# Kernel tuning notes

Measured on AMD Instinct MI355X. Metric: run time of the kernel, lower is better.

## Reference

```python
import jax, jax.numpy as jnp
import numpy as np

DIM, M_DIM, FOURIER, KNN = 128, 16, 4, 32
EDGE_IN = 2 * FOURIER + 2 * DIM + 1  # 265


def silu(x):
    return x * jax.nn.sigmoid(x)


def setup_inputs() -> dict:
    key = jax.random.key(0)
    ks = jax.random.split(key, 12)
    b, n = 2, 4096

    def w(k, shape):
        return jax.random.normal(k, shape, dtype=jnp.float32) * 0.02

    return {
        "feats": jax.random.normal(ks[0], (b, n, DIM), dtype=jnp.float32),
        "coors": jax.random.normal(ks[1], (b, n, 3), dtype=jnp.float32) * 3.0,
        # edge_mlp: Linear(265, 530) -> SiLU -> Linear(530, 16) -> SiLU
        "We1": w(ks[2], (EDGE_IN, 2 * EDGE_IN)), "be1": jnp.zeros((2 * EDGE_IN,), jnp.float32),
        "We2": w(ks[3], (2 * EDGE_IN, M_DIM)), "be2": jnp.zeros((M_DIM,), jnp.float32),
        # coors_mlp: Linear(16, 64) -> SiLU -> Linear(64, 1)
        "Wc1": w(ks[4], (M_DIM, 4 * M_DIM)), "bc1": jnp.zeros((4 * M_DIM,), jnp.float32),
        "Wc2": w(ks[5], (4 * M_DIM, 1)), "bc2": jnp.zeros((1,), jnp.float32),
        # node_mlp: Linear(dim+16, 2*dim) -> SiLU -> Linear(2*dim, dim)
        "Wn1": w(ks[6], (DIM + M_DIM, 2 * DIM)), "bn1": jnp.zeros((2 * DIM,), jnp.float32),
        "Wn2": w(ks[7], (2 * DIM, DIM)), "bn2": jnp.zeros((DIM,), jnp.float32),
    }


def reference(feats, coors, We1, be1, We2, be2, Wc1, bc1, Wc2, bc2, Wn1, bn1, Wn2, bn2):
    b, n, d = feats.shape
    # pairwise relative coords and squared distance: (b, n, n, 3), (b, n, n)
    rel_coors = coors[:, :, None, :] - coors[:, None, :, :]
    rel_dist = jnp.sum(rel_coors ** 2, axis=-1)

    # k nearest neighbors (smallest distance)
    _, idx = jax.lax.top_k(-rel_dist, KNN)  # (b, n, K)
    rel_coors = jnp.take_along_axis(rel_coors, idx[..., None], axis=2)  # (b, n, K, 3)
    rel_dist = jnp.take_along_axis(rel_dist, idx, axis=2)[..., None]    # (b, n, K, 1)

    # fourier encode distance -> (b, n, K, 2*F + 1)
    scales = 2.0 ** jnp.arange(FOURIER, dtype=rel_dist.dtype)
    xs = rel_dist[..., None] / scales  # (b, n, K, 1, F)
    fe = jnp.concatenate([jnp.sin(xs), jnp.cos(xs), rel_dist[..., None]], axis=-1)
    rel_dist = fe.reshape(b, n, KNN, 2 * FOURIER + 1)

    bidx = jnp.arange(b)[:, None, None]
    feats_j = feats[bidx, idx]                                   # (b, n, K, d)
    feats_i = jnp.broadcast_to(feats[:, :, None, :], (b, n, KNN, d))

    edge_in = jnp.concatenate([feats_i, feats_j, rel_dist], axis=-1)  # (b, n, K, 265)
    m_ij = silu(silu(edge_in @ We1 + be1) @ We2 + be2)                # (b, n, K, m)

    coor_w = (silu(m_ij @ Wc1 + bc1) @ Wc2 + bc2)[..., 0]             # (b, n, K)
    coors_out = jnp.einsum('bij,bijc->bic', coor_w, rel_coors) + coors

    m_i = m_ij.sum(axis=2)                                            # (b, n, m)
    node_h = silu(jnp.concatenate([feats, m_i], axis=-1) @ Wn1 + bn1)
    node_out = node_h @ Wn2 + bn2 + feats
    return node_out, coors_out
```

## Files before the change

kernel.cpp:

```cpp
#include <hip/hip_runtime.h>
#include <hip/hip_bf16.h>
#include <stdint.h>

typedef __hip_bfloat16 bf16;

using sh8    = __attribute__((ext_vector_type(8)))  short;
using sh4    = __attribute__((ext_vector_type(4)))  short;
using us4    = __attribute__((ext_vector_type(4)))  unsigned short;
using f32x16 = __attribute__((ext_vector_type(16))) float;
using fx4    = __attribute__((ext_vector_type(4)))  float;
using i32x2  = __attribute__((ext_vector_type(2)))  int;

#define NN    4096
#define NODES 8192
#define DIM   128
#define MD    16
#define KNNK  32
#define H1N   530
#define CPAD  544
#define PROW  1088

#define OFF_W1AB 0
#define OFF_WE2A 8704
#define OFF_WC1A 17536
#define OFF_BE2  19584
#define OFF_BC1  19616
#define OFF_WC2  19744
#define OFF_BC2  19872
#define WIMG_SH  19880

__device__ __forceinline__ float b2f(bf16 x){ return __bfloat162float(x); }
__device__ __forceinline__ bf16  f2b(float x){ return __float2bfloat16(x); }
__device__ __forceinline__ float silu_f(float x){
    return x * __builtin_amdgcn_rcpf(1.f + __expf(-x));
}

__device__ __forceinline__ unsigned short f2us(float f){
    unsigned x = __float_as_uint(f);
    unsigned r = x + 0x7FFFu + ((x >> 16) & 1u);
    return (unsigned short)(r >> 16);
}
__device__ __forceinline__ float us2f(unsigned short u){
    return __uint_as_float(((unsigned)u) << 16);
}
__device__ __forceinline__ unsigned pkbf(float a, float b){
    __hip_bfloat162 v = __float22bfloat162_rn(make_float2(a, b));
    return *(unsigned*)&v;
}
__device__ __forceinline__ void plswap(unsigned &a, unsigned &b){
    i32x2 r = __builtin_amdgcn_permlane32_swap((int)a, (int)b, false, false);
    a = (unsigned)r[0]; b = (unsigned)r[1];
}
__device__ __forceinline__ sh8 mk8(unsigned a, unsigned b, unsigned c, unsigned d){
    union { unsigned u[4]; sh8 s; } x;
    x.u[0] = a; x.u[1] = b; x.u[2] = c; x.u[3] = d;
    return x.s;
}
__device__ __forceinline__ float ldconv(const void* p, int fl, size_t i){
    return fl ? ((const float*)p)[i] : b2f(((const bf16*)p)[i]);
}

struct Ptrs { const void* p[14]; int n[14]; };

__global__ __launch_bounds__(256) void detect_kernel(Ptrs ps, int* flags){
    int tn = blockIdx.x;
    const bf16* s = (const bf16*)ps.p[tn];
    int n = ps.n[tn]; if (n > 8192) n = 8192;
    int bad = 0;
    for (int i = threadIdx.x; i < n; i += 256){
        float v = b2f(s[i]);
        if (!(fabsf(v) <= 64.f)) bad = 1;
    }
    __shared__ int sbad;
    if (threadIdx.x == 0) sbad = 0;
    __syncthreads();
    if (bad) atomicOr(&sbad, 1);
    __syncthreads();
    if (threadIdx.x == 0) flags[tn] = sbad;
}

#define PREP_TOTAL 1340352
__global__ __launch_bounds__(256) void prep_all(Ptrs ps, const int* __restrict__ flags,
        unsigned short* __restrict__ gwimg, unsigned short* __restrict__ We1T,
        unsigned short* __restrict__ fBF,   float* __restrict__ coorsF,
        float* __restrict__ be1F,  float* __restrict__ Wn1F,
        float* __restrict__ bn1F,  float* __restrict__ Wn2F,
        float* __restrict__ bn2F,  float* __restrict__ coorsS){
    int gid = blockIdx.x * 256 + threadIdx.x;
    if (gid < 4352){
        int c = gid >> 3, f = gid & 7;
        gwimg[OFF_W1AB + gid] =
            (c < H1N) ? f2us(ldconv(ps.p[2], flags[2], (size_t)(256 + f) * H1N + c)) : 0;
    } else if (gid < 8704){
        int e = gid - 4352; int c = e >> 3, jj = e & 7;
        gwimg[OFF_W1AB + 4352 + e] =
            (jj == 0 && c < H1N) ? f2us(ldconv(ps.p[2], flags[2], (size_t)264 * H1N + c)) : 0;
    } else if (gid < 17536){
        int e = gid - 8704; int o = e / 552, c = e - o * 552;
        gwimg[OFF_WE2A + e] =
            (c < H1N) ? f2us(ldconv(ps.p[4], flags[4], (size_t)c * 16 + o)) : 0;
    } else if (gid < 19584){
        int e = gid - 17536; int u = e >> 5, k = e & 31;
        gwimg[OFF_WC1A + e] =
            (k < 16) ? f2us(ldconv(ps.p[6], flags[6], (size_t)k * 64 + u)) : 0;
    } else if (gid < 19600){
        ((float*)(gwimg + OFF_BE2))[gid - 19584] = ldconv(ps.p[5], flags[5], gid - 19584);
    } else if (gid < 19664){
        ((float*)(gwimg + OFF_BC1))[gid - 19600] = ldconv(ps.p[7], flags[7], gid - 19600);
    } else if (gid < 19728){
        ((float*)(gwimg + OFF_WC2))[gid - 19664] = ldconv(ps.p[8], flags[8], gid - 19664);
    } else if (gid < 19732){
        int z = gid - 19728;
        ((float*)(gwimg + OFF_BC2))[z] = (z == 0) ? ldconv(ps.p[9], flags[9], 0) : 0.f;
    } else if (gid >= 32768 && gid < 172032){
        int e = gid - 32768; int n = e >> 7, k = e & 127;
        float v;
        if (n < CPAD) v = (n < H1N) ? ldconv(ps.p[2], flags[2], (size_t)k * H1N + n) : 0.f;
        else { int n2 = n - CPAD;
               v = (n2 < H1N) ? ldconv(ps.p[2], flags[2], (size_t)(128 + k) * H1N + n2) : 0.f; }
        We1T[e] = f2us(v);
    } else if (gid >= 172032 && gid < 1220608){
        int e = gid - 172032;
        fBF[e] = f2us(ldconv(ps.p[0], flags[0], e));
    } else if (gid >= 1220608 && gid < 1245184){
        int e = gid - 1220608;
        coorsF[e] = ldconv(ps.p[1], flags[1], e);
    } else if (gid >= 1245184 && gid < 1245714){
        int e = gid - 1245184;
        be1F[e] = ldconv(ps.p[3], flags[3], e);
    } else if (gid >= 1245760 && gid < 1282624){
        int e = gid - 1245760;
        Wn1F[e] = ldconv(ps.p[10], flags[10], e);
    } else if (gid >= 1282624 && gid < 1282880){
        int e = gid - 1282624;
        bn1F[e] = ldconv(ps.p[11], flags[11], e);
    } else if (gid >= 1282880 && gid < 1315648){
        int e = gid - 1282880;
        Wn2F[e] = ldconv(ps.p[12], flags[12], e);
    } else if (gid >= 1315648 && gid < 1315776){
        int e = gid - 1315648;
        bn2F[e] = ldconv(ps.p[13], flags[13], e);
    } else if (gid >= 1315776 && gid < 1340352){
        int e = gid - 1315776;
        int n = e / 3, c = e - n * 3;
        coorsS[(size_t)c * NODES + n] = ldconv(ps.p[1], flags[1], e);
    }
}

__global__ __launch_bounds__(512, 6) void knn_kernel(const float* __restrict__ coorsS,
                                                     int* __restrict__ idx_out){
    __shared__ unsigned hist[8][1024];
    __shared__ unsigned long long blist[8][64];
    __shared__ int cntO[8], cntB[8];

    int t = threadIdx.x, lane = t & 63, wid = t >> 6;
    int node = (blockIdx.x << 3) + wid;
    int b = node >> 12, i = node & (NN - 1);
    const float* cx = coorsS + (size_t)b * NN;
    const float* cy = coorsS + NODES + (size_t)b * NN;
    const float* cz = coorsS + 2 * NODES + (size_t)b * NN;

    float qx = cx[i], qy = cy[i], qz = cz[i];

    unsigned* h = &hist[wid][0];
    {
        uint4* hz = (uint4*)h;
        uint4 z = make_uint4(0,0,0,0);
        #pragma unroll
        for (int zl = 0; zl < 4; ++zl) hz[zl * 64 + lane] = z;
    }
    if (lane == 0){ cntO[wid] = 0; cntB[wid] = 0; }
    asm volatile("" ::: "memory");

    for (int s = 0; s < 16; ++s){
        int j0 = (s << 8) + (lane << 2);
        fx4 X = *(const fx4*)(cx + j0);
        fx4 Y = *(const fx4*)(cy + j0);
        fx4 Z = *(const fx4*)(cz + j0);
        #pragma unroll
        for (int k = 0; k < 4; ++k){
            float dx = qx - X[k], dy = qy - Y[k], dz = qz - Z[k];
            float d  = dx*dx + dy*dy + dz*dz;
            float d2 = d * d;
            atomicAdd(&h[__float_as_uint(d2 * d2) >> 22], 1u);
        }
    }
    asm volatile("s_waitcnt lgkmcnt(0)" ::: "memory");

    unsigned S = 0;
    {
        uint4* hz = (uint4*)h;
        #pragma unroll
        for (int g = 0; g < 4; ++g){
            uint4 v = hz[lane * 4 + g];
            S += v.x + v.y + v.z + v.w;
        }
    }
    unsigned scan = S;
    #pragma unroll
    for (int off = 1; off < 64; off <<= 1){
        unsigned nv = __shfl_up(scan, off);
        if (lane >= off) scan += nv;
    }
    unsigned excl = scan - S;
    unsigned long long own = __ballot(excl < KNNK && excl + S >= KNNK);
    int src = __ffsll((unsigned long long)own) - 1;
    unsigned run = excl, Bloc = 0, below_l = 0;
    #pragma unroll
    for (int r = 0; r < 16; ++r){
        unsigned c = h[lane * 16 + r];
        if (run < KNNK && run + c >= KNNK){ Bloc = lane * 16 + r; below_l = run; }
        run += c;
    }
    unsigned B    = __shfl(Bloc, src);
    unsigned below= __shfl(below_l, src);
    unsigned need = KNNK - below;

    int* co = &cntO[wid];
    int* cbn = &cntB[wid];
    unsigned long long* bl = &blist[wid][0];
    for (int s = 0; s < 16; ++s){
        int j0 = (s << 8) + (lane << 2);
        fx4 X = *(const fx4*)(cx + j0);
        fx4 Y = *(const fx4*)(cy + j0);
        fx4 Z = *(const fx4*)(cz + j0);
        #pragma unroll
        for (int k = 0; k < 4; ++k){
            float dx = qx - X[k], dy = qy - Y[k], dz = qz - Z[k];
            float d  = dx*dx + dy*dy + dz*dz;
            float d2 = d * d;
            unsigned bk = __float_as_uint(d2 * d2) >> 22;
            int j = j0 + k;
            if (bk < B){
                int pos = atomicAdd(co, 1);
                idx_out[(size_t)node * KNNK + pos] = j;
            } else if (bk == B){
                unsigned long long mk = ((unsigned long long)__float_as_uint(d) << 32)
                                        | (unsigned)j;
                int p = atomicAdd(cbn, 1);
                if (p < 64) bl[p] = mk;
            }
        }
    }
    asm volatile("s_waitcnt lgkmcnt(0) vmcnt(0)" ::: "memory");
    int nb = *cbn;

    if (nb <= 64){
        unsigned long long e = (lane < nb) ? bl[lane] : ~0ull;
        for (unsigned r = 0; r < need; ++r){
            unsigned long long m = e;
            #pragma unroll
            for (int off = 32; off > 0; off >>= 1){
                unsigned long long o = __shfl_xor(m, off);
                if (o < m) m = o;
            }
            if (lane == 0)
                idx_out[(size_t)node * KNNK + below + r] = (int)(unsigned)(m & 0xffffffffull);
            if (e == m) e = ~0ull;
        }
    } else {
        unsigned long long lastk = 0;
        for (unsigned r = 0; r < need; ++r){
            unsigned long long lmin = ~0ull;
            for (int s = 0; s < 64; ++s){
                int j = (s << 6) + lane;
                float dx = qx - cx[j];
                float dy = qy - cy[j];
                float dz = qz - cz[j];
                float d  = dx*dx + dy*dy + dz*dz;
                float d2 = d * d;
                if ((__float_as_uint(d2 * d2) >> 22) == B){
                    unsigned long long mk = (((unsigned long long)__float_as_uint(d) << 32)
                                             | (unsigned)j) + 1ull;
                    if (mk > lastk && mk < lmin) lmin = mk;
                }
            }
            #pragma unroll
            for (int off = 32; off > 0; off >>= 1){
                unsigned long long o = __shfl_xor(lmin, off);
                if (o < lmin) lmin = o;
            }
            if (lane == 0)
                idx_out[(size_t)node * KNNK + below + r] =
                    (int)(unsigned)((lmin - 1ull) & 0xffffffffull);
            lastk = lmin;
        }
    }
}

__global__ __launch_bounds__(256) void p_gemm(const unsigned short* __restrict__ fBF,
                                              const unsigned short* __restrict__ We1T,
                                              const float* __restrict__ be1,
                                              unsigned short* __restrict__ P){
    int t = threadIdx.x, lane = t & 63, wid = t >> 6;
    int e31 = lane & 31, hi = lane >> 5;
    int mW = (blockIdx.x << 7) + (wid << 5);
    int n0 = blockIdx.y << 5;

    const unsigned short* Arow = fBF  + (size_t)(mW + e31) * DIM + hi * 8;
    const unsigned short* Brow = We1T + (size_t)(n0 + e31) * DIM + hi * 8;

    f32x16 acc = {0.f,0.f,0.f,0.f,0.f,0.f,0.f,0.f,0.f,0.f,0.f,0.f,0.f,0.f,0.f,0.f};
    #pragma unroll
    for (int kc = 0; kc < 8; ++kc){
        sh8 a  = *(const sh8*)(Arow + kc * 16);
        sh8 bv = *(const sh8*)(Brow + kc * 16);
        acc = __builtin_amdgcn_mfma_f32_32x32x16_bf16(a, bv, acc, 0, 0, 0);
    }
    int n = n0 + e31;
    float beadd = 0.f;
    if (n < CPAD) beadd = (n < H1N) ? be1[n] : 0.f;
    #pragma unroll
    for (int g = 0; g < 4; ++g)
        #pragma unroll
        for (int r = 0; r < 4; ++r){
            int m = mW + 8*g + 4*hi + r;
            P[(size_t)m * PROW + n] = f2us(acc[4*g + r] + beadd);
        }
}

__global__ __launch_bounds__(512, 6) void edge_kernel(
        const float* __restrict__ coors, const int* __restrict__ idx,
        const unsigned short* __restrict__ gw,
        const unsigned short* __restrict__ P,
        float* __restrict__ mi_out, void* __restrict__ dout,
        const int* __restrict__ flagp){
    __shared__ __align__(16) unsigned short sWe2[16 * 552];
    __shared__ __align__(16) unsigned short trans[8][1280];

    int t = threadIdx.x, lane = t & 63, wid = t >> 6;
    int gnode = (blockIdx.x << 3) + wid;
    int b = gnode >> 12;

    {
        const float4* s1 = (const float4*)(gw + OFF_WE2A);
        float4* d1 = (float4*)sWe2;
        for (int e = t; e < 1104; e += 512) d1[e] = s1[e];
    }

    const float* cb = coors + (size_t)b * NN * 3;
    int i = gnode & (NN - 1);
    float qx = cb[i*3+0], qy = cb[i*3+1], qz = cb[i*3+2];

    int e31 = lane & 31, hi = lane >> 5;
    int e15 = lane & 15, q  = lane >> 4;

    int jme = idx[(size_t)gnode * KNNK + e31];
    float rx = qx - cb[jme*3+0];
    float ry = qy - cb[jme*3+1];
    float rz = qz - cb[jme*3+2];
    float d = rx*rx + ry*ry + rz*rz;

    float s8v, c8v;
    __sincosf(d * 0.125f, &s8v, &c8v);
    float s4  = 2.f*s8v*c8v, c4  = 1.f - 2.f*s8v*s8v;
    float s2a = 2.f*s4*c4,   c2a = 1.f - 2.f*s4*s4;
    float s1a = 2.f*s2a*c2a, c1a = 1.f - 2.f*s2a*s2a;

    unsigned frb[9];
    frb[0] = f2us(s1a); frb[1] = f2us(s2a); frb[2] = f2us(s4); frb[3] = f2us(s8v);
    frb[4] = f2us(c1a); frb[5] = f2us(c2a); frb[6] = f2us(c4); frb[7] = f2us(c8v);
    frb[8] = f2us(d);

    sh8 bfragC;
    #pragma unroll
    for (int j = 0; j < 8; ++j)
        bfragC[j] = (hi == 0) ? (short)frb[j]
                  : (short)((j == 0) ? frb[8] : (j == 1) ? 0x3F80u : 0u);

    int nbase = gnode & ~(NN - 1);
    int j0 = __shfl(jme, lane >> 2);
    int j1 = __shfl(jme, 16 + (lane >> 2));
    const unsigned short* Pst0 = P + (size_t)(nbase + j0) * PROW + CPAD + (lane & 3) * 8;
    const unsigned short* Pst1 = P + (size_t)(nbase + j1) * PROW + CPAD + (lane & 3) * 8;
    const unsigned short* Pirow = P + (size_t)gnode * PROW;

    unsigned short* stg = &trans[wid][0];
    unsigned short* sw0 = stg + (lane >> 2) * 40 + (lane & 3) * 8;
    unsigned short* sw1 = stg + (16 + (lane >> 2)) * 40 + (lane & 3) * 8;

    const float* g_be2 = (const float*)(gw + OFF_BE2);
    const float* g_bc1 = (const float*)(gw + OFF_BC1);
    const float* g_wc2 = (const float*)(gw + OFF_WC2);
    const float* g_bc2 = (const float*)(gw + OFF_BC2);

    f32x16 accD = {0.f,0.f,0.f,0.f,0.f,0.f,0.f,0.f,
                   0.f,0.f,0.f,0.f,0.f,0.f,0.f,0.f};

    sh8 g0v = *(const sh8*)(Pst0);
    sh8 g1v = *(const sh8*)(Pst1);

    __syncthreads();

    #pragma unroll 1
    for (int ch = 0; ch < 17; ++ch){
        int c0 = ch * 32;
        *(sh8*)sw0 = g0v;
        *(sh8*)sw1 = g1v;
        if (ch < 16){
            g0v = *(const sh8*)(Pst0 + c0 + 32);
            g1v = *(const sh8*)(Pst1 + c0 + 32);
        }

        unsigned short piS = Pirow[c0 + e31];
        sh8 afrag = *(const sh8*)(gw + OFF_W1AB + (size_t)(hi * 544 + c0 + e31) * 8);
        afrag[1] = hi ? (short)piS : afrag[1];

        f32x16 cc;
        #pragma unroll
        for (int g = 0; g < 4; ++g){
            us4 pj = *(const us4*)(stg + e31 * 40 + 8*g + 4*hi);
            cc[4*g+0] = us2f(pj.x);
            cc[4*g+1] = us2f(pj.y);
            cc[4*g+2] = us2f(pj.z);
            cc[4*g+3] = us2f(pj.w);
        }
        f32x16 h = __builtin_amdgcn_mfma_f32_32x32x16_bf16(afrag, bfragC, cc, 0, 0, 0);

        unsigned u0 = pkbf(silu_f(h[0]),  silu_f(h[1]));
        unsigned u1 = pkbf(silu_f(h[2]),  silu_f(h[3]));
        unsigned u2 = pkbf(silu_f(h[4]),  silu_f(h[5]));
        unsigned u3 = pkbf(silu_f(h[6]),  silu_f(h[7]));
        unsigned u4 = pkbf(silu_f(h[8]),  silu_f(h[9]));
        unsigned u5 = pkbf(silu_f(h[10]), silu_f(h[11]));
        unsigned u6 = pkbf(silu_f(h[12]), silu_f(h[13]));
        unsigned u7 = pkbf(silu_f(h[14]), silu_f(h[15]));
        plswap(u0, u2); plswap(u1, u3);
        plswap(u4, u6); plswap(u5, u7);
        sh8 A1 = mk8(u0, u1, u2, u3);
        sh8 A2 = mk8(u4, u5, u6, u7);

        const unsigned short* wrow = &sWe2[(size_t)(e31 & 15) * 552 + c0 + (hi << 3)];
        sh8 B1 = *(const sh8*)(wrow);
        sh8 B2 = *(const sh8*)(wrow + 16);
        accD = __builtin_amdgcn_mfma_f32_32x32x16_bf16(A1, B1, accD, 0, 0, 0);
        accD = __builtin_amdgcn_mfma_f32_32x32x16_bf16(A2, B2, accD, 0, 0, 0);
    }

    float be2v = g_be2[e31 & 15];
    float mval[16];
    float msum = 0.f;
    #pragma unroll
    for (int r = 0; r < 16; ++r){
        mval[r] = silu_f(accD[r] + be2v);
        msum += mval[r];
    }
    msum += __shfl_xor(msum, 32);

    if (e31 < 16){
        #pragma unroll
        for (int r = 0; r < 16; ++r){
            int edge = (r & 3) + 8 * (r >> 2) + 4 * hi;
            stg[edge * 16 + e31] = f2us(mval[r]);
        }
        if (hi == 0)
            mi_out[(size_t)gnode * MD + e31] = msum;
    }

    float tsum0 = 0.f, tsum1 = 0.f;
    #pragma unroll
    for (int ut = 0; ut < 4; ++ut){
        sh8 wa3 = *(const sh8*)(gw + OFF_WC1A + (size_t)(ut * 16 + e15) * 32 + q * 8);
        sh8 b0  = (q < 2) ? *(const sh8*)&stg[e15 * 16 + q * 8]        : (sh8)0;
        sh8 b1  = (q < 2) ? *(const sh8*)&stg[(16 + e15) * 16 + q * 8] : (sh8)0;
        fx4 a0 = {0.f,0.f,0.f,0.f};
        fx4 a1 = {0.f,0.f,0.f,0.f};
        a0 = __builtin_amdgcn_mfma_f32_16x16x32_bf16(wa3, b0, a0, 0, 0, 0);
        a1 = __builtin_amdgcn_mfma_f32_16x16x32_bf16(wa3, b1, a1, 0, 0, 0);
        fx4 bc1q = *(const fx4*)&g_bc1[ut * 16 + q * 4];
        fx4 wcq  = *(const fx4*)&g_wc2[ut * 16 + q * 4];
        #pragma unroll
        for (int r = 0; r < 4; ++r){
            tsum0 += silu_f(a0[r] + bc1q[r]) * wcq[r];
            tsum1 += silu_f(a1[r] + bc1q[r]) * wcq[r];
        }
    }
    tsum0 += __shfl_xor(tsum0, 16); tsum0 += __shfl_xor(tsum0, 32);
    tsum1 += __shfl_xor(tsum1, 16); tsum1 += __shfl_xor(tsum1, 32);
    float cw = ((lane < 16) ? tsum0 : tsum1) + g_bc2[0];

    float en = (lane < 32) ? 1.f : 0.f;
    float cx = en * cw * rx, cy = en * cw * ry, cz = en * cw * rz;
    #pragma unroll
    for (int off = 1; off <= 32; off <<= 1){
        cx += __shfl_xor(cx, off);
        cy += __shfl_xor(cy, off);
        cz += __shfl_xor(cz, off);
    }
    if (lane == 0){
        size_t base = (size_t)NODES * DIM + (size_t)gnode * 3;
        if (*flagp){
            float* o = (float*)dout;
            o[base+0] = cx + qx; o[base+1] = cy + qy; o[base+2] = cz + qz;
        } else {
            bf16* o = (bf16*)dout;
            o[base+0] = f2b(cx + qx); o[base+1] = f2b(cy + qy); o[base+2] = f2b(cz + qz);
        }
    }
}

__global__ __launch_bounds__(256) void node_kernel(
        const void* __restrict__ featsRaw, const float* __restrict__ m_i,
        const float* __restrict__ Wn1,   const float* __restrict__ bn1,
        const float* __restrict__ Wn2,   const float* __restrict__ bn2,
        void* __restrict__ dout,         const int* __restrict__ flagp){
    __shared__ __align__(16) float X[8][144];
    __shared__ __align__(16) float Hs[8][256];
    int t = threadIdx.x;
    int g0 = blockIdx.x << 3;
    int fl = flagp[0];

    for (int e = t; e < 8 * DIM; e += 256){
        int nd = e >> 7, c = e & 127;
        size_t off = (size_t)(g0 + nd) * DIM + c;
        X[nd][c] = fl ? ((const float*)featsRaw)[off]
                      : b2f(((const bf16*)featsRaw)[off]);
    }
    if (t < 128){
        int nd = t >> 4, c = t & 15;
        X[nd][DIM + c] = m_i[(size_t)(g0 + nd) * MD + c];
    }
    __syncthreads();

    float acc[8] = {};
    for (int r4 = 0; r4 < 144; r4 += 4){
        float w0 = Wn1[(size_t)(r4+0) * 256 + t];
        float w1 = Wn1[(size_t)(r4+1) * 256 + t];
        float w2 = Wn1[(size_t)(r4+2) * 256 + t];
        float w3 = Wn1[(size_t)(r4+3) * 256 + t];
        #pragma unroll
        for (int nd = 0; nd < 8; ++nd){
            fx4 x4 = *(const fx4*)&X[nd][r4];
            acc[nd] += x4[0]*w0 + x4[1]*w1 + x4[2]*w2 + x4[3]*w3;
        }
    }
    float bb = bn1[t];
    #pragma unroll
    for (int nd = 0; nd < 8; ++nd) Hs[nd][t] = silu_f(acc[nd] + bb);
    __syncthreads();

    int c = t & 127, g = t >> 7;
    float a2[4] = {};
    for (int r4 = 0; r4 < 256; r4 += 4){
        float w0 = Wn2[(size_t)(r4+0) * DIM + c];
        float w1 = Wn2[(size_t)(r4+1) * DIM + c];
        float w2 = Wn2[(size_t)(r4+2) * DIM + c];
        float w3 = Wn2[(size_t)(r4+3) * DIM + c];
        #pragma unroll
        for (int u = 0; u < 4; ++u){
            fx4 h4 = *(const fx4*)&Hs[g*4 + u][r4];
            a2[u] += h4[0]*w0 + h4[1]*w1 + h4[2]*w2 + h4[3]*w3;
        }
    }
    float b2v = bn2[c];
    #pragma unroll
    for (int u = 0; u < 4; ++u){
        int nd = g*4 + u;
        float v = a2[u] + b2v + X[nd][c];
        size_t off2 = (size_t)(g0 + nd) * DIM + c;
        if (fl) ((float*)dout)[off2] = v;
        else    ((bf16*)dout)[off2]  = f2b(v);
    }
}

extern "C" void kernel_launch(void* const* d_in, const int* in_sizes, int n_in,
                              void* d_out, int out_size, void* d_ws, size_t ws_size,
                              hipStream_t stream){
    char* ws = (char*)d_ws;
    size_t off = 0;
    auto alloc = [&](size_t bytes) -> char* {
        off = (off + 511) & ~(size_t)511;
        char* p = ws + off;
        off += bytes;
        return p;
    };

    int* flags = (int*)alloc(14 * 4);
    unsigned short* gwimg = (unsigned short*)alloc((size_t)WIMG_SH * 2);
    unsigned short* We1T  = (unsigned short*)alloc((size_t)1088 * 128 * 2);
    unsigned short* fBF   = (unsigned short*)alloc((size_t)NODES * DIM * 2);
    float* coorsF = (float*)alloc((size_t)2 * NN * 3 * 4);
    float* be1F   = (float*)alloc((size_t)544 * 4);
    float* Wn1F   = (float*)alloc((size_t)144 * 256 * 4);
    float* bn1F   = (float*)alloc((size_t)256 * 4);
    float* Wn2F   = (float*)alloc((size_t)256 * 128 * 4);
    float* bn2F   = (float*)alloc((size_t)128 * 4);
    float* coorsS = (float*)alloc((size_t)3 * NODES * 4);
    int*   idx    = (int*)  alloc((size_t)NODES * KNNK * 4);
    unsigned short* P = (unsigned short*) alloc((size_t)NODES * PROW * 2);
    float* mi     = (float*)alloc((size_t)NODES * MD * 4);

    Ptrs ps;
    for (int i = 0; i < 14; ++i){ ps.p[i] = d_in[i]; ps.n[i] = in_sizes[i]; }

    detect_kernel<<<14, 256, 0, stream>>>(ps, flags);
    prep_all<<<(PREP_TOTAL + 255) / 256, 256, 0, stream>>>(
        ps, flags, gwimg, We1T, fBF, coorsF, be1F, Wn1F, bn1F, Wn2F, bn2F, coorsS);
    knn_kernel<<<NODES/8, 512, 0, stream>>>(coorsS, idx);
    p_gemm<<<dim3(64, 34), 256, 0, stream>>>(fBF, We1T, be1F, P);
    edge_kernel<<<NODES/8, 512, 0, stream>>>(coorsF, idx, gwimg, P, mi,
                                             d_out, flags + 0);
    node_kernel<<<1024, 256, 0, stream>>>(d_in[0], mi, Wn1F, bn1F, Wn2F, bn2F,
                                          d_out, flags + 0);
}
```

Measured before the change: 252.0 us.

## Stage kNN coordinates in LDS, swizzle edge staging, enlarge node-MLP tiles

The kNN kernel now copies the batch's coordinates into shared memory once per block and reads them from there. It also halves the histogram to 512 buckets (shift by 23) and lowers the launch-bounds occupancy hint. The edge kernel XOR-swizzles its transpose staging buffer to avoid LDS bank conflicts. The node kernel processes 32 nodes per block instead of 8, so each weight load is reused four times more, at the cost of more registers and fewer blocks. Coarser buckets may send more candidates to the boundary-bucket path, including the slow fallback.

```diff
diff --git a/kernel.cpp b/kernel.cpp
--- a/kernel.cpp
+++ b/kernel.cpp
@@ -147,30 +147,38 @@
     }
 }
 
-__global__ __launch_bounds__(512, 6) void knn_kernel(const float* __restrict__ coorsS,
+__global__ __launch_bounds__(512, 4) void knn_kernel(const float* __restrict__ coorsS,
                                                      int* __restrict__ idx_out){
-    __shared__ unsigned hist[8][1024];
+    __shared__ __align__(16) float sC[3 * NN];
+    __shared__ unsigned hist[8][512];
     __shared__ unsigned long long blist[8][64];
     __shared__ int cntO[8], cntB[8];
 
     int t = threadIdx.x, lane = t & 63, wid = t >> 6;
     int node = (blockIdx.x << 3) + wid;
-    int b = node >> 12, i = node & (NN - 1);
-    const float* cx = coorsS + (size_t)b * NN;
-    const float* cy = coorsS + NODES + (size_t)b * NN;
-    const float* cz = coorsS + 2 * NODES + (size_t)b * NN;
-
+    int b = blockIdx.x >> 9;
+    int i = node & (NN - 1);
+
+    {
+        for (int e = t; e < 3072; e += 512){
+            int pl = e >> 10, i4 = e & 1023;
+            ((fx4*)sC)[e] = *((const fx4*)(coorsS + (size_t)pl * NODES + (size_t)b * NN) + i4);
+        }
+    }
+    if (lane == 0){ cntO[wid] = 0; cntB[wid] = 0; }
+    {
+        uint4* hz = (uint4*)&hist[wid][0];
+        uint4 z = make_uint4(0,0,0,0);
+        hz[lane] = z; hz[64 + lane] = z;
+    }
+    __syncthreads();
+
+    const float* cx = sC;
+    const float* cy = sC + NN;
+    const float* cz = sC + 2 * NN;
     float qx = cx[i], qy = cy[i], qz = cz[i];
 
     unsigned* h = &hist[wid][0];
-    {
-        uint4* hz = (uint4*)h;
-        uint4 z = make_uint4(0,0,0,0);
-        #pragma unroll
-        for (int zl = 0; zl < 4; ++zl) hz[zl * 64 + lane] = z;
-    }
-    if (lane == 0){ cntO[wid] = 0; cntB[wid] = 0; }
-    asm volatile("" ::: "memory");
 
     for (int s = 0; s < 16; ++s){
         int j0 = (s << 8) + (lane << 2);
@@ -182,7 +190,7 @@
             float dx = qx - X[k], dy = qy - Y[k], dz = qz - Z[k];
             float d  = dx*dx + dy*dy + dz*dz;
             float d2 = d * d;
-            atomicAdd(&h[__float_as_uint(d2 * d2) >> 22], 1u);
+            atomicAdd(&h[__float_as_uint(d2 * d2) >> 23], 1u);
         }
     }
     asm volatile("s_waitcnt lgkmcnt(0)" ::: "memory");
@@ -191,8 +199,8 @@
     {
         uint4* hz = (uint4*)h;
         #pragma unroll
-        for (int g = 0; g < 4; ++g){
-            uint4 v = hz[lane * 4 + g];
+        for (int g = 0; g < 2; ++g){
+            uint4 v = hz[lane * 2 + g];
             S += v.x + v.y + v.z + v.w;
         }
     }
@@ -207,9 +215,9 @@
     int src = __ffsll((unsigned long long)own) - 1;
     unsigned run = excl, Bloc = 0, below_l = 0;
     #pragma unroll
-    for (int r = 0; r < 16; ++r){
-        unsigned c = h[lane * 16 + r];
-        if (run < KNNK && run + c >= KNNK){ Bloc = lane * 16 + r; below_l = run; }
+    for (int r = 0; r < 8; ++r){
+        unsigned c = h[lane * 8 + r];
+        if (run < KNNK && run + c >= KNNK){ Bloc = lane * 8 + r; below_l = run; }
         run += c;
     }
     unsigned B    = __shfl(Bloc, src);
@@ -229,7 +237,7 @@
             float dx = qx - X[k], dy = qy - Y[k], dz = qz - Z[k];
             float d  = dx*dx + dy*dy + dz*dz;
             float d2 = d * d;
-            unsigned bk = __float_as_uint(d2 * d2) >> 22;
+            unsigned bk = __float_as_uint(d2 * d2) >> 23;
             int j = j0 + k;
             if (bk < B){
                 int pos = atomicAdd(co, 1);
@@ -269,7 +277,7 @@
                 float dz = qz - cz[j];
                 float d  = dx*dx + dy*dy + dz*dz;
                 float d2 = d * d;
-                if ((__float_as_uint(d2 * d2) >> 22) == B){
+                if ((__float_as_uint(d2 * d2) >> 23) == B){
                     unsigned long long mk = (((unsigned long long)__float_as_uint(d) << 32)
                                              | (unsigned)j) + 1ull;
                     if (mk > lastk && mk < lmin) lmin = mk;
@@ -376,8 +384,9 @@
     const unsigned short* Pirow = P + (size_t)gnode * PROW;
 
     unsigned short* stg = &trans[wid][0];
-    unsigned short* sw0 = stg + (lane >> 2) * 40 + (lane & 3) * 8;
-    unsigned short* sw1 = stg + (16 + (lane >> 2)) * 40 + (lane & 3) * 8;
+    int r0 = lane >> 2, r1 = 16 + (lane >> 2), qq = lane & 3;
+    unsigned short* sw0 = stg + r0 * 40 + ((qq ^ (r0 >> 3)) << 3);
+    unsigned short* sw1 = stg + r1 * 40 + ((qq ^ (r1 >> 3)) << 3);
 
     const float* g_be2 = (const float*)(gw + OFF_BE2);
     const float* g_bc1 = (const float*)(gw + OFF_BC1);
@@ -389,6 +398,9 @@
 
     sh8 g0v = *(const sh8*)(Pst0);
     sh8 g1v = *(const sh8*)(Pst1);
+
+    int sx = e31 >> 3;
+    const unsigned short* ccb = stg + e31 * 40 + 4 * hi;
 
     __syncthreads();
 
@@ -409,7 +421,7 @@
         f32x16 cc;
         #pragma unroll
         for (int g = 0; g < 4; ++g){
-            us4 pj = *(const us4*)(stg + e31 * 40 + 8*g + 4*hi);
+            us4 pj = *(const us4*)(ccb + ((g ^ sx) << 3));
             cc[4*g+0] = us2f(pj.x);
             cc[4*g+1] = us2f(pj.y);
             cc[4*g+2] = us2f(pj.z);
@@ -480,21 +492,21 @@
     float cw = ((lane < 16) ? tsum0 : tsum1) + g_bc2[0];
 
     float en = (lane < 32) ? 1.f : 0.f;
-    float cx = en * cw * rx, cy = en * cw * ry, cz = en * cw * rz;
+    float cx2 = en * cw * rx, cy2 = en * cw * ry, cz2 = en * cw * rz;
     #pragma unroll
     for (int off = 1; off <= 32; off <<= 1){
-        cx += __shfl_xor(cx, off);
-        cy += __shfl_xor(cy, off);
-        cz += __shfl_xor(cz, off);
+        cx2 += __shfl_xor(cx2, off);
+        cy2 += __shfl_xor(cy2, off);
+        cz2 += __shfl_xor(cz2, off);
     }
     if (lane == 0){
         size_t base = (size_t)NODES * DIM + (size_t)gnode * 3;
         if (*flagp){
             float* o = (float*)dout;
-            o[base+0] = cx + qx; o[base+1] = cy + qy; o[base+2] = cz + qz;
+            o[base+0] = cx2 + qx; o[base+1] = cy2 + qy; o[base+2] = cz2 + qz;
         } else {
             bf16* o = (bf16*)dout;
-            o[base+0] = f2b(cx + qx); o[base+1] = f2b(cy + qy); o[base+2] = f2b(cz + qz);
+            o[base+0] = f2b(cx2 + qx); o[base+1] = f2b(cy2 + qy); o[base+2] = f2b(cz2 + qz);
         }
     }
 }
@@ -504,62 +516,66 @@
         const float* __restrict__ Wn1,   const float* __restrict__ bn1,
         const float* __restrict__ Wn2,   const float* __restrict__ bn2,
         void* __restrict__ dout,         const int* __restrict__ flagp){
-    __shared__ __align__(16) float X[8][144];
-    __shared__ __align__(16) float Hs[8][256];
+    __shared__ __align__(16) float X[32][144];
+    __shared__ __align__(16) float Hs[32][256];
     int t = threadIdx.x;
-    int g0 = blockIdx.x << 3;
+    int g0 = blockIdx.x << 5;
     int fl = flagp[0];
 
-    for (int e = t; e < 8 * DIM; e += 256){
+    for (int e = t; e < 32 * DIM; e += 256){
         int nd = e >> 7, c = e & 127;
         size_t off = (size_t)(g0 + nd) * DIM + c;
         X[nd][c] = fl ? ((const float*)featsRaw)[off]
                       : b2f(((const bf16*)featsRaw)[off]);
     }
-    if (t < 128){
-        int nd = t >> 4, c = t & 15;
+    for (int e = t; e < 32 * MD; e += 256){
+        int nd = e >> 4, c = e & 15;
         X[nd][DIM + c] = m_i[(size_t)(g0 + nd) * MD + c];
     }
     __syncthreads();
 
-    float acc[8] = {};
-    for (int r4 = 0; r4 < 144; r4 += 4){
-        float w0 = Wn1[(size_t)(r4+0) * 256 + t];
-        float w1 = Wn1[(size_t)(r4+1) * 256 + t];
-        float w2 = Wn1[(size_t)(r4+2) * 256 + t];
-        float w3 = Wn1[(size_t)(r4+3) * 256 + t];
-        #pragma unroll
-        for (int nd = 0; nd < 8; ++nd){
-            fx4 x4 = *(const fx4*)&X[nd][r4];
-            acc[nd] += x4[0]*w0 + x4[1]*w1 + x4[2]*w2 + x4[3]*w3;
-        }
-    }
-    float bb = bn1[t];
-    #pragma unroll
-    for (int nd = 0; nd < 8; ++nd) Hs[nd][t] = silu_f(acc[nd] + bb);
+    {
+        float acc[32] = {};
+        for (int r4 = 0; r4 < 144; r4 += 4){
+            float w0 = Wn1[(size_t)(r4+0) * 256 + t];
+            float w1 = Wn1[(size_t)(r4+1) * 256 + t];
+            float w2 = Wn1[(size_t)(r4+2) * 256 + t];
+            float w3 = Wn1[(size_t)(r4+3) * 256 + t];
+            #pragma unroll
+            for (int nd = 0; nd < 32; ++nd){
+                fx4 x4 = *(const fx4*)&X[nd][r4];
+                acc[nd] += x4[0]*w0 + x4[1]*w1 + x4[2]*w2 + x4[3]*w3;
+            }
+        }
+        float bb = bn1[t];
+        #pragma unroll
+        for (int nd = 0; nd < 32; ++nd) Hs[nd][t] = silu_f(acc[nd] + bb);
+    }
     __syncthreads();
 
-    int c = t & 127, g = t >> 7;
-    float a2[4] = {};
-    for (int r4 = 0; r4 < 256; r4 += 4){
-        float w0 = Wn2[(size_t)(r4+0) * DIM + c];
-        float w1 = Wn2[(size_t)(r4+1) * DIM + c];
-        float w2 = Wn2[(size_t)(r4+2) * DIM + c];
-        float w3 = Wn2[(size_t)(r4+3) * DIM + c];
-        #pragma unroll
-        for (int u = 0; u < 4; ++u){
-            fx4 h4 = *(const fx4*)&Hs[g*4 + u][r4];
-            a2[u] += h4[0]*w0 + h4[1]*w1 + h4[2]*w2 + h4[3]*w3;
-        }
-    }
-    float b2v = bn2[c];
-    #pragma unroll
-    for (int u = 0; u < 4; ++u){
-        int nd = g*4 + u;
-        float v = a2[u] + b2v + X[nd][c];
-        size_t off2 = (size_t)(g0 + nd) * DIM + c;
-        if (fl) ((float*)dout)[off2] = v;
-        else    ((bf16*)dout)[off2]  = f2b(v);
+    {
+        int c = t & 127, gg = t >> 7;
+        float a2[16] = {};
+        for (int r4 = 0; r4 < 256; r4 += 4){
+            float w0 = Wn2[(size_t)(r4+0) * DIM + c];
+            float w1 = Wn2[(size_t)(r4+1) * DIM + c];
+            float w2 = Wn2[(size_t)(r4+2) * DIM + c];
+            float w3 = Wn2[(size_t)(r4+3) * DIM + c];
+            #pragma unroll
+            for (int u = 0; u < 16; ++u){
+                fx4 h4 = *(const fx4*)&Hs[gg*16 + u][r4];
+                a2[u] += h4[0]*w0 + h4[1]*w1 + h4[2]*w2 + h4[3]*w3;
+            }
+        }
+        float b2v = bn2[c];
+        #pragma unroll
+        for (int u = 0; u < 16; ++u){
+            int nd = gg*16 + u;
+            float v = a2[u] + b2v + X[nd][c];
+            size_t off2 = (size_t)(g0 + nd) * DIM + c;
+            if (fl) ((float*)dout)[off2] = v;
+            else    ((bf16*)dout)[off2]  = f2b(v);
+        }
     }
 }
 
@@ -600,6 +616,6 @@
     p_gemm<<<dim3(64, 34), 256, 0, stream>>>(fBF, We1T, be1F, P);
     edge_kernel<<<NODES/8, 512, 0, stream>>>(coorsF, idx, gwimg, P, mi,
                                              d_out, flags + 0);
-    node_kernel<<<1024, 256, 0, stream>>>(d_in[0], mi, Wn1F, bn1F, Wn2F, bn2F,
-                                          d_out, flags + 0);
-}
+    node_kernel<<<256, 256, 0, stream>>>(d_in[0], mi, Wn1F, bn1F, Wn2F, bn2F,
+                                         d_out, flags + 0);
+}
```

New measurement: 303.6 us. +20.5%, slower.
